# Kernel optimization log

Measured on AMD Instinct MI355X. Metric: run time of the kernel, lower is better.

## Reference

```python
import jax, jax.numpy as jnp
import numpy as np
from jax import lax

B, C_IN, C_OUT, T = 2048, 64, 64, 32
E = 32768
K_HOPS = 2
KSIZE = 3
EPS = 1e-5
SLOPE = 0.01  # torch LeakyReLU default negative_slope


def setup_inputs() -> dict:
    key = jax.random.key(0)
    ks = jax.random.split(key, 10)
    x = jax.random.normal(ks[0], (B, C_IN, T), dtype=jnp.float32)
    edge_index = jax.random.randint(ks[1], (2, E), 0, B, dtype=jnp.int64)
    edge_weight = jax.random.uniform(ks[2], (E,), dtype=jnp.float32)
    # temporal Conv1d params: weight [out, in, k], bias [out]
    conv_w = jax.random.normal(ks[3], (C_OUT, C_IN, KSIZE), dtype=jnp.float32) / np.sqrt(C_IN * KSIZE)
    conv_b = jnp.zeros((C_OUT,), dtype=jnp.float32)
    # LayerNorm([out_channels, T]) elementwise affine over last two dims
    ln_g = jnp.ones((C_OUT, T), dtype=jnp.float32)
    ln_b = jnp.zeros((C_OUT, T), dtype=jnp.float32)
    # BatchNorm1d over node features inside residual layer (res+ pre-norm)
    bn_g = jnp.ones((C_OUT,), dtype=jnp.float32)
    bn_b = jnp.zeros((C_OUT,), dtype=jnp.float32)
    # TAGConv: one linear per hop (K+1 of them) plus bias
    tag_w = jax.random.normal(ks[4], (K_HOPS + 1, C_OUT, C_OUT), dtype=jnp.float32) / np.sqrt(C_OUT)
    tag_b = jnp.zeros((C_OUT,), dtype=jnp.float32)
    return {
        'x': x, 'edge_index': edge_index, 'edge_weight': edge_weight,
        'conv_w': conv_w, 'conv_b': conv_b, 'ln_g': ln_g, 'ln_b': ln_b,
        'bn_g': bn_g, 'bn_b': bn_b, 'tag_w': tag_w, 'tag_b': tag_b,
    }


def _forward(x, edge_index, edge_weight, conv_w, conv_b, ln_g, ln_b, bn_g, bn_b, tag_w, tag_b):
    Bn, Cin, Tn = x.shape
    # --- Temporal1DConvLayer: Conv1d with padding=k-1 both sides, truncate to T, pool='none', LeakyReLU ---
    y = lax.conv_general_dilated(x, conv_w, window_strides=(1,),
                                 padding=[(KSIZE - 1, KSIZE - 1)],
                                 dimension_numbers=('NCH', 'OIH', 'NCH'))
    y = y + conv_b[None, :, None]
    y = y[..., :Tn]                                   # [B, C_out, T]
    y = jnp.where(y >= 0, y, SLOPE * y)               # LeakyReLU
    # --- temporal_norm_layer: LayerNorm over (C_out, T) jointly ---
    mu = jnp.mean(y, axis=(1, 2), keepdims=True)
    var = jnp.var(y, axis=(1, 2), keepdims=True)
    y = (y - mu) * lax.rsqrt(var + EPS) * ln_g[None] + ln_b[None]
    # --- parallelize over time: permute(2,0,1) -> [T, B, F]; edges replicated per t ---
    h_in = jnp.transpose(y, (2, 0, 1))                # [T, B, F]
    # --- ResidualLayer (res+): h = h_in + TAGConv(LeakyReLU(BatchNorm(h_in))) ---
    mu_n = jnp.mean(h_in, axis=(0, 1))                # batch stats over all T*B node copies
    var_n = jnp.var(h_in, axis=(0, 1))
    z = (h_in - mu_n) * lax.rsqrt(var_n + EPS) * bn_g + bn_b
    z = jnp.where(z >= 0, z, SLOPE * z)
    src, dst = edge_index[0], edge_index[1]
    out = jnp.einsum('tbf,fg->tbg', z, tag_w[0])
    p = z
    for k in range(1, K_HOPS + 1):
        msg = p[:, src, :] * edge_weight[None, :, None]   # [T, E, F] gather
        p = jnp.zeros_like(p).at[:, dst, :].add(msg)      # scatter-add per timestep
        out = out + jnp.einsum('tbf,fg->tbg', p, tag_w[k])
    out = out + tag_b
    h = h_in + out                                    # residual 'res+'
    # --- reshape back: [T, B, F] -> [B, F, T] ---
    return jnp.transpose(h, (1, 2, 0))


def reference(x, edge_index, edge_weight, conv_w, conv_b, ln_g, ln_b, bn_g, bn_b, tag_w, tag_b):
    return _forward(x, edge_index, edge_weight, conv_w, conv_b, ln_g, ln_b, bn_g, bn_b, tag_w, tag_b)
```

## Files before the change

kernel.cpp:

```cpp
#include <hip/hip_runtime.h>
#include <cstddef>

#define NB   2048
#define NE   32768
#define NTC  2048
#define SLOPE_F 0.01f
#define EPS_F   1e-5f

typedef short bf16x8 __attribute__((ext_vector_type(8)));
typedef float f32x4  __attribute__((ext_vector_type(4)));

__device__ __forceinline__ unsigned short f2bf(float f) {
    unsigned u = __builtin_bit_cast(unsigned, f);
    u += 0x7FFF + ((u >> 16) & 1);
    return (unsigned short)(u >> 16);
}
__device__ __forceinline__ float bflo(unsigned v) {
    return __builtin_bit_cast(float, v << 16);
}
__device__ __forceinline__ float bfhi(unsigned v) {
    return __builtin_bit_cast(float, v & 0xFFFF0000u);
}
__device__ __forceinline__ unsigned pk2(float lo, float hi) {
    return (unsigned)f2bf(lo) | ((unsigned)f2bf(hi) << 16);
}
__device__ __forceinline__ void accv8(float* acc, const uint4& v, float wt) {
    acc[0] += wt * bflo(v.x); acc[1] += wt * bfhi(v.x);
    acc[2] += wt * bflo(v.y); acc[3] += wt * bfhi(v.y);
    acc[4] += wt * bflo(v.z); acc[5] += wt * bfhi(v.z);
    acc[6] += wt * bflo(v.w); acc[7] += wt * bfhi(v.w);
}
__device__ __forceinline__ void acci16(float* acc, const uint4& v, float wt) {
    acc[0] += wt * (float)(short)(v.x & 0xFFFFu); acc[1] += wt * (float)(short)(v.x >> 16);
    acc[2] += wt * (float)(short)(v.y & 0xFFFFu); acc[3] += wt * (float)(short)(v.y >> 16);
    acc[4] += wt * (float)(short)(v.z & 0xFFFFu); acc[5] += wt * (float)(short)(v.z >> 16);
    acc[6] += wt * (float)(short)(v.w & 0xFFFFu); acc[7] += wt * (float)(short)(v.w >> 16);
}
__device__ __forceinline__ unsigned pkq2(float a, float b, float inv) {
    int qa = __float2int_rn(a * inv);
    int qb = __float2int_rn(b * inv);
    return ((unsigned)qa & 0xFFFFu) | ((unsigned)qb << 16);
}

__device__ __forceinline__ int edge_src(const int* ei, int m, int e) {
    return m ? ei[e] : ei[2 * e];
}
__device__ __forceinline__ int edge_dst(const int* ei, int m, int e) {
    return m ? ei[NE + e] : ei[2 * (NE + e)];
}

__global__ __launch_bounds__(256)
void k_hist(const int* __restrict__ ei, int* __restrict__ hist,
            const float* __restrict__ cw, unsigned short* __restrict__ wAb,
            const float* __restrict__ tw, unsigned short* __restrict__ twB)
{
    int e = blockIdx.x * 256 + threadIdx.x;
    unsigned long long bal = __ballot(ei[2 * e + 1] != 0);
    int m = (bal != 0ull) ? 1 : 0;
    atomicAdd(&hist[edge_dst(ei, m, e)], 1);
    if (blockIdx.x < 48) {
        int idx = e;
        int kk = idx >> 12, o = (idx >> 6) & 63, i = idx & 63;
        wAb[idx] = f2bf(cw[o * 192 + i * 3 + kk]);
    } else if (blockIdx.x < 96) {
        int idx = e - 48 * 256;
        int mm = idx >> 12, rem = idx & 4095;
        int g = rem >> 6, k = rem & 63;
        twB[idx] = f2bf(tw[mm * 4096 + k * 64 + g]);
    }
}

__global__ __launch_bounds__(256)
void k_scan(const int* __restrict__ hist, int* __restrict__ rowp, int* __restrict__ cur)
{
    __shared__ int part[256];
    int j = threadIdx.x;
    int loc[8]; int s = 0;
#pragma unroll
    for (int r = 0; r < 8; ++r) { loc[r] = hist[j * 8 + r]; s += loc[r]; }
    part[j] = s;
    __syncthreads();
    for (int off = 1; off < 256; off <<= 1) {
        int v = (j >= off) ? part[j - off] : 0;
        __syncthreads();
        part[j] += v;
        __syncthreads();
    }
    int excl = part[j] - s;
#pragma unroll
    for (int r = 0; r < 8; ++r) {
        rowp[j * 8 + r] = excl;
        cur [j * 8 + r] = excl;
        excl += loc[r];
    }
    if (j == 255) rowp[2048] = excl;
}

__global__ __launch_bounds__(256)
void k_scat(const int* __restrict__ ei, const float* __restrict__ ew,
            int* __restrict__ cur, int* __restrict__ csrs, float* __restrict__ csrw)
{
    int e = blockIdx.x * 256 + threadIdx.x;
    unsigned long long bal = __ballot(ei[2 * e + 1] != 0);
    int m = (bal != 0ull) ? 1 : 0;
    int d = edge_dst(ei, m, e);
    int pos = atomicAdd(&cur[d], 1);
    csrs[pos] = edge_src(ei, m, e);
    csrw[pos] = ew[e];
}

__global__ __launch_bounds__(256, 4)
void k_convln(const float* __restrict__ x, const unsigned short* __restrict__ wAb,
              const float* __restrict__ cb, const float* __restrict__ lg,
              const float* __restrict__ lb, float* __restrict__ h_in,
              float* __restrict__ partials)
{
    __shared__ __align__(16) unsigned short xT[36 * 72];
    __shared__ float hT[32 * 65];
    __shared__ float red1[64], red2[64];
    __shared__ float wsum[8];
    __shared__ float bcast[2];

    const int b = blockIdx.x, j = threadIdx.x;
    const float* __restrict__ xg = x + (size_t)b * NTC;

    {
        unsigned* xTd = (unsigned*)xT;
        int t = j & 31, p = j >> 5;
#pragma unroll
        for (int r = 0; r < 4; ++r) {
            int i0 = (r * 8 + p) * 2;
            float v0 = xg[i0 * 32 + t];
            float v1 = xg[(i0 + 1) * 32 + t];
            xTd[(t + 2) * 36 + (i0 >> 1)] = pk2(v0, v1);
        }
        if (j < 72)       xTd[j] = 0u;
        else if (j < 144) xTd[1224 + (j - 72)] = 0u;
    }
    __syncthreads();

    const int lane = j & 63, w = j >> 6;
    const int n16 = lane & 15, quad = lane >> 4;

    bf16x8 afr[3][2];
#pragma unroll
    for (int kk = 0; kk < 3; ++kk)
#pragma unroll
        for (int s = 0; s < 2; ++s) {
            int off16 = (kk * 64 + w * 16 + n16) * 64 + s * 32 + quad * 8;
            afr[kk][s] = *(const bf16x8*)(wAb + off16);
        }

    f32x4 acc0 = {0.f, 0.f, 0.f, 0.f};
    f32x4 acc1 = {0.f, 0.f, 0.f, 0.f};
#pragma unroll
    for (int kk = 0; kk < 3; ++kk)
#pragma unroll
        for (int s = 0; s < 2; ++s) {
            bf16x8 b0 = *(const bf16x8*)(xT + (n16 + kk) * 72 + s * 32 + quad * 8);
            bf16x8 b1 = *(const bf16x8*)(xT + (16 + n16 + kk) * 72 + s * 32 + quad * 8);
            acc0 = __builtin_amdgcn_mfma_f32_16x16x32_bf16(afr[kk][s], b0, acc0, 0, 0, 0);
            acc1 = __builtin_amdgcn_mfma_f32_16x16x32_bf16(afr[kk][s], b1, acc1, 0, 0, 0);
        }

    float vals[2][4];
    float s1 = 0.f, s2 = 0.f;
#pragma unroll
    for (int r = 0; r < 4; ++r) {
        float cbv = cb[w * 16 + quad * 4 + r];
        float v0 = acc0[r] + cbv;
        float v1 = acc1[r] + cbv;
        v0 = (v0 >= 0.f) ? v0 : SLOPE_F * v0;
        v1 = (v1 >= 0.f) ? v1 : SLOPE_F * v1;
        vals[0][r] = v0; vals[1][r] = v1;
        s1 += v0 + v1; s2 += v0 * v0 + v1 * v1;
    }
#pragma unroll
    for (int off = 32; off > 0; off >>= 1) {
        s1 += __shfl_down(s1, off, 64);
        s2 += __shfl_down(s2, off, 64);
    }
    if (lane == 0) { wsum[w] = s1; wsum[4 + w] = s2; }
    __syncthreads();
    if (j == 0) {
        float S1 = wsum[0] + wsum[1] + wsum[2] + wsum[3];
        float S2 = wsum[4] + wsum[5] + wsum[6] + wsum[7];
        float mu  = S1 * (1.f / 2048.f);
        float var = S2 * (1.f / 2048.f) - mu * mu;
        bcast[0] = mu;
        bcast[1] = rsqrtf(var + EPS_F);
    }
    __syncthreads();
    const float mu = bcast[0], rs = bcast[1];
    float po1[4] = {0.f, 0.f, 0.f, 0.f}, po2[4] = {0.f, 0.f, 0.f, 0.f};
#pragma unroll
    for (int nt = 0; nt < 2; ++nt) {
        int t = nt * 16 + n16;
#pragma unroll
        for (int r = 0; r < 4; ++r) {
            int o = w * 16 + quad * 4 + r;
            float h = (vals[nt][r] - mu) * rs * lg[o * 32 + t] + lb[o * 32 + t];
            hT[t * 65 + o] = h;
            po1[r] += h; po2[r] += h * h;
        }
    }
#pragma unroll
    for (int off = 8; off > 0; off >>= 1) {
#pragma unroll
        for (int r = 0; r < 4; ++r) {
            po1[r] += __shfl_down(po1[r], off, 16);
            po2[r] += __shfl_down(po2[r], off, 16);
        }
    }
    if (n16 == 0) {
#pragma unroll
        for (int r = 0; r < 4; ++r) {
            int o = w * 16 + quad * 4 + r;
            red1[o] = po1[r];
            red2[o] = po2[r];
        }
    }
    __syncthreads();
    float* hb = h_in + (size_t)b * NTC;
#pragma unroll
    for (int r = 0; r < 8; ++r) {
        int idx = j + r * 256;
        hb[idx] = hT[(idx >> 6) * 65 + (idx & 63)];
    }
    float* pb_ = partials + (size_t)b * 128;
    if (j < 64)       pb_[j] = red1[j];
    else if (j < 128) pb_[j] = red2[j - 64];
}

__global__ __launch_bounds__(256)
void k_bnred(const float* __restrict__ partials, const float* __restrict__ bg,
             const float* __restrict__ bb, float* __restrict__ stats)
{
    const int c = blockIdx.x, j = threadIdx.x;
    float s1 = 0.f, s2 = 0.f;
    for (int b = j; b < NB; b += 256) {
        const float* p = partials + (size_t)b * 128;
        s1 += p[c];
        s2 += p[64 + c];
    }
    __shared__ float r1[4], r2[4];
#pragma unroll
    for (int off = 32; off > 0; off >>= 1) {
        s1 += __shfl_down(s1, off, 64);
        s2 += __shfl_down(s2, off, 64);
    }
    if ((j & 63) == 0) { r1[j >> 6] = s1; r2[j >> 6] = s2; }
    __syncthreads();
    if (j == 0) {
        float S1 = r1[0] + r1[1] + r1[2] + r1[3];
        float S2 = r2[0] + r2[1] + r2[2] + r2[3];
        const float inv_n = 1.f / 65536.f;
        float mu  = S1 * inv_n;
        float var = S2 * inv_n - mu * mu;
        float rs  = rsqrtf(var + EPS_F);
        float sc  = bg[c] * rs;
        stats[128 + c] = sc;
        stats[192 + c] = bb[c] - mu * sc;
    }
}

__global__ __launch_bounds__(256)
void k_zlite(const float* __restrict__ h_in, const float* __restrict__ stats,
             unsigned short* __restrict__ zb16)
{
    __shared__ float scs[64], shs[64];
    const int b = blockIdx.x, j = threadIdx.x;
    if (j < 64)        scs[j] = stats[128 + j];
    else if (j < 128)  shs[j - 64] = stats[192 + (j - 64)];
    __syncthreads();
    const float4* hb = (const float4*)(h_in + (size_t)b * NTC);
    float4 a = hb[2 * j], c4 = hb[2 * j + 1];
    const int c0 = (j * 8) & 63;
    float z0 = a.x  * scs[c0+0] + shs[c0+0];
    float z1 = a.y  * scs[c0+1] + shs[c0+1];
    float z2 = a.z  * scs[c0+2] + shs[c0+2];
    float z3 = a.w  * scs[c0+3] + shs[c0+3];
    float z4 = c4.x * scs[c0+4] + shs[c0+4];
    float z5 = c4.y * scs[c0+5] + shs[c0+5];
    float z6 = c4.z * scs[c0+6] + shs[c0+6];
    float z7 = c4.w * scs[c0+7] + shs[c0+7];
    z0 = (z0 >= 0.f) ? z0 : SLOPE_F * z0;  z1 = (z1 >= 0.f) ? z1 : SLOPE_F * z1;
    z2 = (z2 >= 0.f) ? z2 : SLOPE_F * z2;  z3 = (z3 >= 0.f) ? z3 : SLOPE_F * z3;
    z4 = (z4 >= 0.f) ? z4 : SLOPE_F * z4;  z5 = (z5 >= 0.f) ? z5 : SLOPE_F * z5;
    z6 = (z6 >= 0.f) ? z6 : SLOPE_F * z6;  z7 = (z7 >= 0.f) ? z7 : SLOPE_F * z7;
    uint4 q;
    q.x = pk2(z0, z1); q.y = pk2(z2, z3); q.z = pk2(z4, z5); q.w = pk2(z6, z7);
    ((uint4*)(zb16 + (size_t)b * NTC))[j] = q;
}

__global__ __launch_bounds__(256, 4)
void k_hop1(const unsigned short* __restrict__ p_in, const float* __restrict__ h_in,
            const int* __restrict__ rowp, const int* __restrict__ csrs,
            const float* __restrict__ csrw, const unsigned short* __restrict__ twB,
            const float* __restrict__ tb,
            unsigned short* __restrict__ p1q, float* __restrict__ p1scl,
            float* __restrict__ out)
{
    __shared__ __align__(16) unsigned short pA[32 * 64];
    __shared__ __align__(16) unsigned short zA[32 * 64];
    __shared__ float hl[32 * 65];
    __shared__ float mred[4];
    const int d = blockIdx.x, j = threadIdx.x;

    {
        uint4 zv = ((const uint4*)(p_in + (size_t)d * NTC))[j];
        ((uint4*)zA)[j] = zv;
        const float4* hb4 = (const float4*)(h_in + (size_t)d * NTC);
        float4 h0 = hb4[2 * j], h1 = hb4[2 * j + 1];
        int tt = j >> 3, c0 = (j & 7) * 8;
        float* q = &hl[tt * 65 + c0];
        q[0] = h0.x; q[1] = h0.y; q[2] = h0.z; q[3] = h0.w;
        q[4] = h1.x; q[5] = h1.y; q[6] = h1.z; q[7] = h1.w;
    }

    const int beg = rowp[d], end = rowp[d + 1];
    float acc[8];
#pragma unroll
    for (int r = 0; r < 8; ++r) acc[r] = 0.f;
    int e = beg;
    for (; e + 8 <= end; e += 8) {
        int   s0 = csrs[e],   s1 = csrs[e+1], s2 = csrs[e+2], s3 = csrs[e+3];
        int   s4 = csrs[e+4], s5 = csrs[e+5], s6 = csrs[e+6], s7 = csrs[e+7];
        float w0 = csrw[e],   w1 = csrw[e+1], w2 = csrw[e+2], w3 = csrw[e+3];
        float w4 = csrw[e+4], w5 = csrw[e+5], w6 = csrw[e+6], w7 = csrw[e+7];
        uint4 v0 = ((const uint4*)(p_in + (size_t)s0 * NTC))[j];
        uint4 v1 = ((const uint4*)(p_in + (size_t)s1 * NTC))[j];
        uint4 v2 = ((const uint4*)(p_in + (size_t)s2 * NTC))[j];
        uint4 v3 = ((const uint4*)(p_in + (size_t)s3 * NTC))[j];
        uint4 v4 = ((const uint4*)(p_in + (size_t)s4 * NTC))[j];
        uint4 v5 = ((const uint4*)(p_in + (size_t)s5 * NTC))[j];
        uint4 v6 = ((const uint4*)(p_in + (size_t)s6 * NTC))[j];
        uint4 v7 = ((const uint4*)(p_in + (size_t)s7 * NTC))[j];
        accv8(acc, v0, w0); accv8(acc, v1, w1);
        accv8(acc, v2, w2); accv8(acc, v3, w3);
        accv8(acc, v4, w4); accv8(acc, v5, w5);
        accv8(acc, v6, w6); accv8(acc, v7, w7);
    }
    for (; e + 2 <= end; e += 2) {
        int s0 = csrs[e],  s1 = csrs[e+1];
        float w0 = csrw[e], w1 = csrw[e+1];
        uint4 v0 = ((const uint4*)(p_in + (size_t)s0 * NTC))[j];
        uint4 v1 = ((const uint4*)(p_in + (size_t)s1 * NTC))[j];
        accv8(acc, v0, w0); accv8(acc, v1, w1);
    }
    if (e < end) {
        int s0 = csrs[e];
        float w0 = csrw[e];
        uint4 v0 = ((const uint4*)(p_in + (size_t)s0 * NTC))[j];
        accv8(acc, v0, w0);
    }

    const int lane = j & 63, w = j >> 6;
    float m = 0.f;
#pragma unroll
    for (int r = 0; r < 8; ++r) m = fmaxf(m, fabsf(acc[r]));
#pragma unroll
    for (int off = 32; off > 0; off >>= 1)
        m = fmaxf(m, __shfl_down(m, off, 64));
    if (lane == 0) mred[w] = m;
    __syncthreads();
    const float mv = fmaxf(fmaxf(mred[0], mred[1]), fmaxf(mred[2], mred[3]));
    const float inv = (mv > 0.f) ? (32767.f / mv) : 0.f;
    if (j == 0) p1scl[d] = mv * (1.f / 32767.f);

    {
        uint4 qv;
        qv.x = pkq2(acc[0], acc[1], inv);
        qv.y = pkq2(acc[2], acc[3], inv);
        qv.z = pkq2(acc[4], acc[5], inv);
        qv.w = pkq2(acc[6], acc[7], inv);
        ((uint4*)(p1q + (size_t)d * NTC))[j] = qv;
    }
    uint4 pv;
    pv.x = pk2(acc[0], acc[1]); pv.y = pk2(acc[2], acc[3]);
    pv.z = pk2(acc[4], acc[5]); pv.w = pk2(acc[6], acc[7]);
    ((uint4*)pA)[j] = pv;
    __syncthreads();

    const int n16 = lane & 15, quad = lane >> 4;
    const int g = w * 16 + n16;

    bf16x8 za00 = *(const bf16x8*)(zA + (n16)      * 64 +      quad * 8);
    bf16x8 za01 = *(const bf16x8*)(zA + (n16)      * 64 + 32 + quad * 8);
    bf16x8 za10 = *(const bf16x8*)(zA + (16 + n16) * 64 +      quad * 8);
    bf16x8 za11 = *(const bf16x8*)(zA + (16 + n16) * 64 + 32 + quad * 8);
    bf16x8 pa00 = *(const bf16x8*)(pA + (n16)      * 64 +      quad * 8);
    bf16x8 pa01 = *(const bf16x8*)(pA + (n16)      * 64 + 32 + quad * 8);
    bf16x8 pa10 = *(const bf16x8*)(pA + (16 + n16) * 64 +      quad * 8);
    bf16x8 pa11 = *(const bf16x8*)(pA + (16 + n16) * 64 + 32 + quad * 8);
    bf16x8 b0w0 = *(const bf16x8*)(twB + g * 64 +      quad * 8);
    bf16x8 b1w0 = *(const bf16x8*)(twB + g * 64 + 32 + quad * 8);
    bf16x8 b0w1 = *(const bf16x8*)(twB + 4096 + g * 64 +      quad * 8);
    bf16x8 b1w1 = *(const bf16x8*)(twB + 4096 + g * 64 + 32 + quad * 8);

    f32x4 d0 = {0.f, 0.f, 0.f, 0.f};
    f32x4 d1 = {0.f, 0.f, 0.f, 0.f};
    d0 = __builtin_amdgcn_mfma_f32_16x16x32_bf16(za00, b0w0, d0, 0, 0, 0);
    d0 = __builtin_amdgcn_mfma_f32_16x16x32_bf16(za01, b1w0, d0, 0, 0, 0);
    d0 = __builtin_amdgcn_mfma_f32_16x16x32_bf16(pa00, b0w1, d0, 0, 0, 0);
    d0 = __builtin_amdgcn_mfma_f32_16x16x32_bf16(pa01, b1w1, d0, 0, 0, 0);
    d1 = __builtin_amdgcn_mfma_f32_16x16x32_bf16(za10, b0w0, d1, 0, 0, 0);
    d1 = __builtin_amdgcn_mfma_f32_16x16x32_bf16(za11, b1w0, d1, 0, 0, 0);
    d1 = __builtin_amdgcn_mfma_f32_16x16x32_bf16(pa10, b0w1, d1, 0, 0, 0);
    d1 = __builtin_amdgcn_mfma_f32_16x16x32_bf16(pa11, b1w1, d1, 0, 0, 0);

    const float tbg = tb[g];
    float* ob = out + (size_t)d * NTC + g * 32;
    {
        float4 v;
        v.x = d0[0] + tbg + hl[(quad * 4 + 0) * 65 + g];
        v.y = d0[1] + tbg + hl[(quad * 4 + 1) * 65 + g];
        v.z = d0[2] + tbg + hl[(quad * 4 + 2) * 65 + g];
        v.w = d0[3] + tbg + hl[(quad * 4 + 3) * 65 + g];
        *(float4*)(ob + quad * 4) = v;
    }
    {
        float4 v;
        v.x = d1[0] + tbg + hl[(16 + quad * 4 + 0) * 65 + g];
        v.y = d1[1] + tbg + hl[(16 + quad * 4 + 1) * 65 + g];
        v.z = d1[2] + tbg + hl[(16 + quad * 4 + 2) * 65 + g];
        v.w = d1[3] + tbg + hl[(16 + quad * 4 + 3) * 65 + g];
        *(float4*)(ob + 16 + quad * 4) = v;
    }
}

__global__ __launch_bounds__(256, 4)
void k_hop2(const unsigned short* __restrict__ p1q, const float* __restrict__ p1scl,
            const int* __restrict__ rowp, const int* __restrict__ csrs,
            const float* __restrict__ csrw, const float* __restrict__ tw,
            float* __restrict__ out)
{
    __shared__ float pl[32 * 65];
    __shared__ __align__(16) float W[64 * 64];
    const int d = blockIdx.x, j = threadIdx.x;
#pragma unroll
    for (int r = 0; r < 16; ++r) { int idx = j + r * 256; W[idx] = tw[idx]; }
    const int beg = rowp[d], end = rowp[d + 1];
    float acc[8];
#pragma unroll
    for (int r = 0; r < 8; ++r) acc[r] = 0.f;
    int e = beg;
    for (; e + 8 <= end; e += 8) {
        int   s0 = csrs[e],   s1 = csrs[e+1], s2 = csrs[e+2], s3 = csrs[e+3];
        int   s4 = csrs[e+4], s5 = csrs[e+5], s6 = csrs[e+6], s7 = csrs[e+7];
        float w0 = csrw[e]   * p1scl[s0];
        float w1 = csrw[e+1] * p1scl[s1];
        float w2 = csrw[e+2] * p1scl[s2];
        float w3 = csrw[e+3] * p1scl[s3];
        float w4 = csrw[e+4] * p1scl[s4];
        float w5 = csrw[e+5] * p1scl[s5];
        float w6 = csrw[e+6] * p1scl[s6];
        float w7 = csrw[e+7] * p1scl[s7];
        uint4 v0 = ((const uint4*)(p1q + (size_t)s0 * NTC))[j];
        uint4 v1 = ((const uint4*)(p1q + (size_t)s1 * NTC))[j];
        uint4 v2 = ((const uint4*)(p1q + (size_t)s2 * NTC))[j];
        uint4 v3 = ((const uint4*)(p1q + (size_t)s3 * NTC))[j];
        uint4 v4 = ((const uint4*)(p1q + (size_t)s4 * NTC))[j];
        uint4 v5 = ((const uint4*)(p1q + (size_t)s5 * NTC))[j];
        uint4 v6 = ((const uint4*)(p1q + (size_t)s6 * NTC))[j];
        uint4 v7 = ((const uint4*)(p1q + (size_t)s7 * NTC))[j];
        acci16(acc, v0, w0); acci16(acc, v1, w1);
        acci16(acc, v2, w2); acci16(acc, v3, w3);
        acci16(acc, v4, w4); acci16(acc, v5, w5);
        acci16(acc, v6, w6); acci16(acc, v7, w7);
    }
    for (; e + 2 <= end; e += 2) {
        int s0 = csrs[e],  s1 = csrs[e+1];
        float w0 = csrw[e]   * p1scl[s0];
        float w1 = csrw[e+1] * p1scl[s1];
        uint4 v0 = ((const uint4*)(p1q + (size_t)s0 * NTC))[j];
        uint4 v1 = ((const uint4*)(p1q + (size_t)s1 * NTC))[j];
        acci16(acc, v0, w0); acci16(acc, v1, w1);
    }
    if (e < end) {
        int s0 = csrs[e];
        float w0 = csrw[e] * p1scl[s0];
        uint4 v0 = ((const uint4*)(p1q + (size_t)s0 * NTC))[j];
        acci16(acc, v0, w0);
    }
    {
        int tt = j >> 3, c0 = (j & 7) * 8;
        float* q = &pl[tt * 65 + c0];
#pragma unroll
        for (int s = 0; s < 8; ++s) q[s] = acc[s];
    }
    __syncthreads();
    const int t = j & 31, gq = (j >> 5) * 8;
    float accm[8];
#pragma unroll
    for (int r = 0; r < 8; ++r) accm[r] = 0.f;
    for (int f = 0; f < 64; ++f) {
        float pv = pl[t * 65 + f];
        const float4* Wr = (const float4*)&W[f * 64 + gq];
        float4 wa = Wr[0], wb = Wr[1];
        accm[0] += pv*wa.x; accm[1] += pv*wa.y; accm[2] += pv*wa.z; accm[3] += pv*wa.w;
        accm[4] += pv*wb.x; accm[5] += pv*wb.y; accm[6] += pv*wb.z; accm[7] += pv*wb.w;
    }
    float* ob = out + (size_t)d * NTC;
#pragma unroll
    for (int r = 0; r < 8; ++r)
        ob[(gq + r) * 32 + t] += accm[r];
}

extern "C" void kernel_launch(void* const* d_in, const int* in_sizes, int n_in,
                              void* d_out, int out_size, void* d_ws, size_t ws_size,
                              hipStream_t stream)
{
    const float* x  = (const float*)d_in[0];
    const int*   ei = (const int*)  d_in[1];
    const float* ew = (const float*)d_in[2];
    const float* cw = (const float*)d_in[3];
    const float* cb = (const float*)d_in[4];
    const float* lg = (const float*)d_in[5];
    const float* lb = (const float*)d_in[6];
    const float* bg = (const float*)d_in[7];
    const float* bb = (const float*)d_in[8];
    const float* tw = (const float*)d_in[9];
    const float* tb = (const float*)d_in[10];
    float* out = (float*)d_out;
    float* ws  = (float*)d_ws;

    float*          h_in  = ws;
    unsigned short* p1q   = (unsigned short*)(ws + 4194304);
    float*          p1scl = ws + 6291456;
    unsigned short* zbf   = (unsigned short*)(ws + 8388608);
    float*          stats = ws + 10485760;
    unsigned short* wAb   = (unsigned short*)(ws + 10486016);
    unsigned short* twB   = (unsigned short*)(ws + 10492160);
    float*          parts = ws + 10498304;
    int*            ib    = (int*)(ws + 10760448);
    int*   hist  = ib;
    int*   rowp  = ib + 2048;
    int*   cur   = ib + 4100;
    int*   csrs  = ib + 6148;
    float* csrw  = (float*)(ib + 38916);

    (void)hipMemsetAsync(hist, 0, 2048 * sizeof(int), stream);

    k_hist   <<<128, 256, 0, stream>>>(ei, hist, cw, wAb, tw, twB);
    k_scan   <<<1,   256, 0, stream>>>(hist, rowp, cur);
    k_scat   <<<128, 256, 0, stream>>>(ei, ew, cur, csrs, csrw);
    k_convln <<<NB,  256, 0, stream>>>(x, wAb, cb, lg, lb, h_in, parts);
    k_bnred  <<<64,  256, 0, stream>>>(parts, bg, bb, stats);
    k_zlite  <<<NB,  256, 0, stream>>>(h_in, stats, zbf);
    k_hop1   <<<NB,  256, 0, stream>>>(zbf, h_in, rowp, csrs, csrw, twB, tb, p1q, p1scl, out);
    k_hop2   <<<NB,  256, 0, stream>>>(p1q, p1scl, rowp, csrs, csrw, tw + 8192, out);
}
```

Measured before the change: 170.1 us.

## Merge CSR build kernels into compute kernels to cut launch count

The memset and the three CSR-construction kernels (histogram, scan, scatter) are folded into the existing conv/LN, BN-reduce and z kernels as extra blocks, and the hist zeroing moves into the weight-conversion kernel. This drops the launch sequence from nine operations to six and lets the graph-build work run alongside dense compute blocks. In exchange, the extra blocks in k_main and k_zs still reserve those kernels' shared memory, and the scan and BN reduction now share one launch.

```diff
diff --git a/kernel.cpp b/kernel.cpp
--- a/kernel.cpp
+++ b/kernel.cpp
@@ -50,71 +50,38 @@
 }
 
 __global__ __launch_bounds__(256)
-void k_hist(const int* __restrict__ ei, int* __restrict__ hist,
-            const float* __restrict__ cw, unsigned short* __restrict__ wAb,
-            const float* __restrict__ tw, unsigned short* __restrict__ twB)
-{
-    int e = blockIdx.x * 256 + threadIdx.x;
-    unsigned long long bal = __ballot(ei[2 * e + 1] != 0);
-    int m = (bal != 0ull) ? 1 : 0;
-    atomicAdd(&hist[edge_dst(ei, m, e)], 1);
+void k_pre(int* __restrict__ hist, const float* __restrict__ cw,
+           unsigned short* __restrict__ wAb, const float* __restrict__ tw,
+           unsigned short* __restrict__ twB)
+{
+    int gid = blockIdx.x * 256 + threadIdx.x;
+    if (gid < 2048) hist[gid] = 0;
     if (blockIdx.x < 48) {
-        int idx = e;
+        int idx = gid;
         int kk = idx >> 12, o = (idx >> 6) & 63, i = idx & 63;
         wAb[idx] = f2bf(cw[o * 192 + i * 3 + kk]);
-    } else if (blockIdx.x < 96) {
-        int idx = e - 48 * 256;
+    } else {
+        int idx = gid - 48 * 256;
         int mm = idx >> 12, rem = idx & 4095;
         int g = rem >> 6, k = rem & 63;
         twB[idx] = f2bf(tw[mm * 4096 + k * 64 + g]);
     }
 }
 
-__global__ __launch_bounds__(256)
-void k_scan(const int* __restrict__ hist, int* __restrict__ rowp, int* __restrict__ cur)
-{
-    __shared__ int part[256];
-    int j = threadIdx.x;
-    int loc[8]; int s = 0;
-#pragma unroll
-    for (int r = 0; r < 8; ++r) { loc[r] = hist[j * 8 + r]; s += loc[r]; }
-    part[j] = s;
-    __syncthreads();
-    for (int off = 1; off < 256; off <<= 1) {
-        int v = (j >= off) ? part[j - off] : 0;
-        __syncthreads();
-        part[j] += v;
-        __syncthreads();
-    }
-    int excl = part[j] - s;
-#pragma unroll
-    for (int r = 0; r < 8; ++r) {
-        rowp[j * 8 + r] = excl;
-        cur [j * 8 + r] = excl;
-        excl += loc[r];
-    }
-    if (j == 255) rowp[2048] = excl;
-}
-
-__global__ __launch_bounds__(256)
-void k_scat(const int* __restrict__ ei, const float* __restrict__ ew,
-            int* __restrict__ cur, int* __restrict__ csrs, float* __restrict__ csrw)
-{
-    int e = blockIdx.x * 256 + threadIdx.x;
-    unsigned long long bal = __ballot(ei[2 * e + 1] != 0);
-    int m = (bal != 0ull) ? 1 : 0;
-    int d = edge_dst(ei, m, e);
-    int pos = atomicAdd(&cur[d], 1);
-    csrs[pos] = edge_src(ei, m, e);
-    csrw[pos] = ew[e];
-}
-
 __global__ __launch_bounds__(256, 4)
-void k_convln(const float* __restrict__ x, const unsigned short* __restrict__ wAb,
-              const float* __restrict__ cb, const float* __restrict__ lg,
-              const float* __restrict__ lb, float* __restrict__ h_in,
-              float* __restrict__ partials)
-{
+void k_main(const float* __restrict__ x, const unsigned short* __restrict__ wAb,
+            const float* __restrict__ cb, const float* __restrict__ lg,
+            const float* __restrict__ lb, float* __restrict__ h_in,
+            float* __restrict__ partials,
+            const int* __restrict__ ei, int* __restrict__ hist)
+{
+    if (blockIdx.x >= NB) {
+        int e = (blockIdx.x - NB) * 256 + threadIdx.x;
+        unsigned long long bal = __ballot(ei[2 * e + 1] != 0);
+        int m = (bal != 0ull) ? 1 : 0;
+        atomicAdd(&hist[edge_dst(ei, m, e)], 1);
+        return;
+    }
     __shared__ __align__(16) unsigned short xT[36 * 72];
     __shared__ float hT[32 * 65];
     __shared__ float red1[64], red2[64];
@@ -233,17 +200,43 @@
 }
 
 __global__ __launch_bounds__(256)
-void k_bnred(const float* __restrict__ partials, const float* __restrict__ bg,
-             const float* __restrict__ bb, float* __restrict__ stats)
-{
-    const int c = blockIdx.x, j = threadIdx.x;
+void k_mid(const int* __restrict__ hist, int* __restrict__ rowp,
+           int* __restrict__ cur, const float* __restrict__ partials,
+           const float* __restrict__ bg, const float* __restrict__ bb,
+           float* __restrict__ stats)
+{
+    __shared__ int part[256];
+    __shared__ float r1[4], r2[4];
+    const int j = threadIdx.x;
+    if (blockIdx.x == 0) {
+        int loc[8]; int s = 0;
+#pragma unroll
+        for (int r = 0; r < 8; ++r) { loc[r] = hist[j * 8 + r]; s += loc[r]; }
+        part[j] = s;
+        __syncthreads();
+        for (int off = 1; off < 256; off <<= 1) {
+            int v = (j >= off) ? part[j - off] : 0;
+            __syncthreads();
+            part[j] += v;
+            __syncthreads();
+        }
+        int excl = part[j] - s;
+#pragma unroll
+        for (int r = 0; r < 8; ++r) {
+            rowp[j * 8 + r] = excl;
+            cur [j * 8 + r] = excl;
+            excl += loc[r];
+        }
+        if (j == 255) rowp[2048] = excl;
+        return;
+    }
+    const int c = blockIdx.x - 1;
     float s1 = 0.f, s2 = 0.f;
     for (int b = j; b < NB; b += 256) {
         const float* p = partials + (size_t)b * 128;
         s1 += p[c];
         s2 += p[64 + c];
     }
-    __shared__ float r1[4], r2[4];
 #pragma unroll
     for (int off = 32; off > 0; off >>= 1) {
         s1 += __shfl_down(s1, off, 64);
@@ -265,11 +258,24 @@
 }
 
 __global__ __launch_bounds__(256)
-void k_zlite(const float* __restrict__ h_in, const float* __restrict__ stats,
-             unsigned short* __restrict__ zb16)
-{
+void k_zs(const float* __restrict__ h_in, const float* __restrict__ stats,
+          unsigned short* __restrict__ zb16,
+          const int* __restrict__ ei, const float* __restrict__ ew,
+          int* __restrict__ cur, int* __restrict__ csrs, float* __restrict__ csrw)
+{
+    const int j = threadIdx.x;
+    if (blockIdx.x >= NB) {
+        int e = (blockIdx.x - NB) * 256 + j;
+        unsigned long long bal = __ballot(ei[2 * e + 1] != 0);
+        int m = (bal != 0ull) ? 1 : 0;
+        int d = edge_dst(ei, m, e);
+        int pos = atomicAdd(&cur[d], 1);
+        csrs[pos] = edge_src(ei, m, e);
+        csrw[pos] = ew[e];
+        return;
+    }
     __shared__ float scs[64], shs[64];
-    const int b = blockIdx.x, j = threadIdx.x;
+    const int b = blockIdx.x;
     if (j < 64)        scs[j] = stats[128 + j];
     else if (j < 128)  shs[j - 64] = stats[192 + (j - 64)];
     __syncthreads();
@@ -540,14 +546,10 @@
     int*   csrs  = ib + 6148;
     float* csrw  = (float*)(ib + 38916);
 
-    (void)hipMemsetAsync(hist, 0, 2048 * sizeof(int), stream);
-
-    k_hist   <<<128, 256, 0, stream>>>(ei, hist, cw, wAb, tw, twB);
-    k_scan   <<<1,   256, 0, stream>>>(hist, rowp, cur);
-    k_scat   <<<128, 256, 0, stream>>>(ei, ew, cur, csrs, csrw);
-    k_convln <<<NB,  256, 0, stream>>>(x, wAb, cb, lg, lb, h_in, parts);
-    k_bnred  <<<64,  256, 0, stream>>>(parts, bg, bb, stats);
-    k_zlite  <<<NB,  256, 0, stream>>>(h_in, stats, zbf);
-    k_hop1   <<<NB,  256, 0, stream>>>(zbf, h_in, rowp, csrs, csrw, twB, tb, p1q, p1scl, out);
-    k_hop2   <<<NB,  256, 0, stream>>>(p1q, p1scl, rowp, csrs, csrw, tw + 8192, out);
-}
+    k_pre  <<<96,       256, 0, stream>>>(hist, cw, wAb, tw, twB);
+    k_main <<<NB + 128, 256, 0, stream>>>(x, wAb, cb, lg, lb, h_in, parts, ei, hist);
+    k_mid  <<<65,       256, 0, stream>>>(hist, rowp, cur, parts, bg, bb, stats);
+    k_zs   <<<NB + 128, 256, 0, stream>>>(h_in, stats, zbf, ei, ew, cur, csrs, csrw);
+    k_hop1 <<<NB,       256, 0, stream>>>(zbf, h_in, rowp, csrs, csrw, twB, tb, p1q, p1scl, out);
+    k_hop2 <<<NB,       256, 0, stream>>>(p1q, p1scl, rowp, csrs, csrw, tw + 8192, out);
+}
```

After: 164.9 us. 3.1% less time.
